# Performance work log

Hardware: AMD Instinct MI355X
Metric: run time of the kernel (lower is better)

Reference implementation:

```python
import jax, jax.numpy as jnp
import numpy as np

HEAD_DIM = 64
N_HEADS = 16
D_MODEL = 2048
SEQ = 2048
BATCH = 1
LAYER_IDX = 12
LN_EPS = 1e-5


def setup_inputs() -> dict:
    key = jax.random.key(0)
    ks = jax.random.split(key, 8)
    s = 0.02
    return {
        "x": jax.random.normal(ks[0], (BATCH, SEQ, D_MODEL), dtype=jnp.float32),
        "W_qkv": jax.random.normal(ks[1], (3 * N_HEADS * 2 * HEAD_DIM, D_MODEL), dtype=jnp.float32) * s,
        "W_o": jax.random.normal(ks[2], (D_MODEL, D_MODEL), dtype=jnp.float32) * s,
        "lambda_q1": jax.random.normal(ks[3], (2 * HEAD_DIM,), dtype=jnp.float32) * 0.1,
        "lambda_k1": jax.random.normal(ks[4], (2 * HEAD_DIM,), dtype=jnp.float32) * 0.1,
        "lambda_q2": jax.random.normal(ks[5], (2 * HEAD_DIM,), dtype=jnp.float32) * 0.1,
        "lambda_k2": jax.random.normal(ks[6], (2 * HEAD_DIM,), dtype=jnp.float32) * 0.1,
        "gn_gamma": jnp.ones((N_HEADS, 2 * HEAD_DIM), dtype=jnp.float32),
        "gn_beta": jnp.zeros((N_HEADS, 2 * HEAD_DIM), dtype=jnp.float32),
    }


def _causal_sdpa(q, k, v, scale):
    # q,k: [B,H,S,d], v: [B,H,S,2d]
    S = q.shape[2]
    scores = jnp.einsum("bhqd,bhkd->bhqk", q, k) * scale
    causal = jnp.tril(jnp.ones((S, S), dtype=bool))
    scores = jnp.where(causal[None, None], scores, jnp.float32(-1e30))
    attn = jax.nn.softmax(scores, axis=-1)
    return jnp.einsum("bhqk,bhkd->bhqd", attn, v)


def reference(x, W_qkv, W_o, lambda_q1, lambda_k1, lambda_q2, lambda_k2, gn_gamma, gn_beta):
    B, S, D = x.shape
    lambda_init = 0.8 - 0.6 * jnp.exp(jnp.float32(-0.3 * LAYER_IDX))
    scale = HEAD_DIM ** -0.5

    qkv = x @ W_qkv.T  # [B,S,6*H*d]
    qkv = qkv.reshape(B, S, 3, N_HEADS, 2 * HEAD_DIM)
    q = jnp.transpose(qkv[:, :, 0], (0, 2, 1, 3))  # [B,H,S,2d]
    k = jnp.transpose(qkv[:, :, 1], (0, 2, 1, 3))
    v = jnp.transpose(qkv[:, :, 2], (0, 2, 1, 3))
    q1, q2 = q[..., :HEAD_DIM], q[..., HEAD_DIM:]
    k1, k2 = k[..., :HEAD_DIM], k[..., HEAD_DIM:]

    lam = jnp.exp(lambda_q1 * lambda_k1) - jnp.exp(lambda_q2 * lambda_k2) + lambda_init  # [2d]

    A1 = _causal_sdpa(q1, k1, v, scale)
    A2 = _causal_sdpa(q2, k2, v, scale)
    out = A1 - lam * A2  # broadcast over value channel [B,H,S,2d]

    # per-head LayerNorm over last dim
    mu = jnp.mean(out, axis=-1, keepdims=True)
    var = jnp.mean((out - mu) ** 2, axis=-1, keepdims=True)
    out = (out - mu) * jax.lax.rsqrt(var + LN_EPS)
    out = out * gn_gamma[None, :, None, :] + gn_beta[None, :, None, :]

    out = out * (1.0 - lambda_init)
    out = jnp.transpose(out, (0, 2, 1, 3)).reshape(B, S, D)
    return out @ W_o.T
```

## Files before the change

kernel.cpp:

```cpp
#include <hip/hip_runtime.h>

typedef short short8 __attribute__((ext_vector_type(8)));
typedef float f32x4 __attribute__((ext_vector_type(4)));
typedef unsigned short u16;
typedef u16 u16x8 __attribute__((ext_vector_type(8)));
typedef u16 u16x4 __attribute__((ext_vector_type(4)));

__device__ static inline u16 f2bf(float f) {
    union { float f; unsigned u; } v; v.f = f;
    unsigned r = v.u + 0x7fffu + ((v.u >> 16) & 1u);
    return (u16)(r >> 16);
}

__global__ __launch_bounds__(256) void cast_kernel(const float* __restrict__ in,
                                                   u16* __restrict__ out, int n) {
    int i = (blockIdx.x * 256 + threadIdx.x) * 4;
    if (i + 3 < n) {
        f32x4 v = *(const f32x4*)&in[i];
        u16x4 o;
        o[0] = f2bf(v[0]); o[1] = f2bf(v[1]); o[2] = f2bf(v[2]); o[3] = f2bf(v[3]);
        *(u16x4*)&out[i] = o;
    }
}

template <int BM, int BN, int MODE, int MINW>
__global__ __launch_bounds__(256, MINW) void gemm_bt(const u16* __restrict__ A,
                                                     const u16* __restrict__ B,
                                                     int M, int N, int K,
                                                     float* __restrict__ C,
                                                     u16* __restrict__ Qo,
                                                     u16* __restrict__ Ko,
                                                     u16* __restrict__ Vo) {
    constexpr int APT = BM * 4 / 256;
    constexpr int BPT = BN * 4 / 256;
    constexpr int MT = BM / 32, NT = BN / 32;
    __shared__ u16 As[BM * 32];
    __shared__ u16 Bs[BN * 32];
    const int tid  = threadIdx.x;
    const int lane = tid & 63, wave = tid >> 6;
    const int quad = lane >> 4, l15 = lane & 15;
    const int wm = wave >> 1, wn = wave & 1;
    const int m0 = blockIdx.y * BM;
    const int n0 = blockIdx.x * BN;

    f32x4 acc[MT][NT] = {};

    const u16* aga[APT];
    const u16* bga[BPT];
#pragma unroll
    for (int i = 0; i < APT; i++) {
        int s = tid + i * 256, r = s >> 2;
        int kg = (s & 3) ^ ((r >> 1) & 3);
        aga[i] = &A[(size_t)(m0 + r) * K + kg * 8];
    }
#pragma unroll
    for (int i = 0; i < BPT; i++) {
        int s = tid + i * 256, r = s >> 2;
        int kg = (s & 3) ^ ((r >> 1) & 3);
        bga[i] = &B[(size_t)(n0 + r) * K + kg * 8];
    }

    u16x8 ast[APT], bst[BPT];
#pragma unroll
    for (int i = 0; i < APT; i++) ast[i] = *(const u16x8*)aga[i];
#pragma unroll
    for (int i = 0; i < BPT; i++) bst[i] = *(const u16x8*)bga[i];

    for (int k0 = 0; k0 < K; k0 += 32) {
        if (k0) __syncthreads();
#pragma unroll
        for (int i = 0; i < APT; i++) *(u16x8*)&As[(tid + i * 256) * 8] = ast[i];
#pragma unroll
        for (int i = 0; i < BPT; i++) *(u16x8*)&Bs[(tid + i * 256) * 8] = bst[i];
        __syncthreads();
        if (k0 + 32 < K) {
#pragma unroll
            for (int i = 0; i < APT; i++) ast[i] = *(const u16x8*)(aga[i] + k0 + 32);
#pragma unroll
            for (int i = 0; i < BPT; i++) bst[i] = *(const u16x8*)(bga[i] + k0 + 32);
        }

        short8 af[MT], bf[NT];
#pragma unroll
        for (int mt = 0; mt < MT; mt++) {
            int row = wm * (BM / 2) + mt * 16 + l15;
            int slot = row * 4 + (quad ^ ((row >> 1) & 3));
            af[mt] = *(const short8*)&As[slot * 8];
        }
#pragma unroll
        for (int nt = 0; nt < NT; nt++) {
            int row = wn * (BN / 2) + nt * 16 + l15;
            int slot = row * 4 + (quad ^ ((row >> 1) & 3));
            bf[nt] = *(const short8*)&Bs[slot * 8];
        }
#pragma unroll
        for (int mt = 0; mt < MT; mt++)
#pragma unroll
            for (int nt = 0; nt < NT; nt++)
                acc[mt][nt] = __builtin_amdgcn_mfma_f32_16x16x32_bf16(af[mt], bf[nt], acc[mt][nt], 0, 0, 0);
    }

    if (MODE == 0) {
#pragma unroll
        for (int mt = 0; mt < MT; mt++)
#pragma unroll
            for (int nt = 0; nt < NT; nt++)
#pragma unroll
                for (int r = 0; r < 4; r++) {
                    int row = m0 + wm * (BM / 2) + mt * 16 + quad * 4 + r;
                    int col = n0 + wn * (BN / 2) + nt * 16 + l15;
                    C[(size_t)row * N + col] = acc[mt][nt][r];
                }
    } else {
        const int comp = n0 >> 11, h = (n0 >> 7) & 15;
        u16* dst = (comp == 0) ? Qo : ((comp == 1) ? Ko : Vo);
        const float sc = (comp == 0) ? 0.18033688f : 1.0f;
#pragma unroll
        for (int mt = 0; mt < MT; mt++)
#pragma unroll
            for (int nt = 0; nt < NT; nt++)
#pragma unroll
                for (int r = 0; r < 4; r++) {
                    int row = m0 + wm * (BM / 2) + mt * 16 + quad * 4 + r;
                    int d = wn * (BN / 2) + nt * 16 + l15;
                    dst[((h * 2048) + row) * 128 + d] = f2bf(acc[mt][nt][r] * sc);
                }
    }
}

__global__ __launch_bounds__(256) void transpose_v(const u16* __restrict__ vb,
                                                   u16* __restrict__ vT) {
    __shared__ u16 T[64 * 136];
    const int s0 = blockIdx.x * 64, h = blockIdx.y;
    const int tid = threadIdx.x;
#pragma unroll
    for (int i = 0; i < 4; i++) {
        int c = tid + i * 256;
        int s = c >> 4, dch = c & 15;
        *(u16x8*)&T[s * 136 + dch * 8] =
            *(const u16x8*)&vb[((h * 2048) + s0 + s) * 128 + dch * 8];
    }
    __syncthreads();
#pragma unroll
    for (int i = 0; i < 4; i++) {
        int c = tid + i * 256;
        int d = c >> 3, sch = c & 7;
        u16x8 o;
#pragma unroll
        for (int j = 0; j < 8; j++) o[j] = T[(sch * 8 + j) * 136 + d];
        *(u16x8*)&vT[((h * 128) + d) * 2048 + s0 + sch * 8] = o;
    }
}

__global__ __launch_bounds__(256, 2) void attn_kernel(const u16* __restrict__ qb,
                                                      const u16* __restrict__ kb,
                                                      const u16* __restrict__ vT,
                                                      float* __restrict__ ob) {
    const int bid = blockIdx.x;
    const int h = bid & 15;
    const int comp = (bid >> 4) & 1;
    const int j = bid >> 5;
    const int J = (j < 8) ? (2 * j + 1) : (30 - 2 * j);
    const int nkt = 2 * J + 2;
    const int q0 = J * 128;
    const int tid = threadIdx.x, lane = tid & 63, wave = tid >> 6;
    const int quad = lane >> 4, l15 = lane & 15;

    __shared__ u16 Ks[64 * 64];
    __shared__ u16 VsT[128 * 64];

    const u16* kb_h = &kb[(size_t)h * 2048 * 128 + comp * 64];
    const u16* vT_h = &vT[(size_t)h * 128 * 2048];

    const int c1 = tid, c2 = tid + 256;
    const int k1key = c1 >> 3, k1dc = ((c1 & 7) ^ k1key) & 7;
    const int k2key = c2 >> 3, k2dc = ((c2 & 7) ^ k2key) & 7;
    const u16* kaddr1 = &kb_h[k1key * 128 + k1dc * 8];
    const u16* kaddr2 = &kb_h[k2key * 128 + k2dc * 8];
    const u16* vaddr[4];
#pragma unroll
    for (int i = 0; i < 4; i++) {
        int c = tid + i * 256;
        int dim = c >> 3, kc = ((c & 7) ^ dim) & 7;
        vaddr[i] = &vT_h[dim * 2048 + kc * 8];
    }

    short8 aq[2][2];
#pragma unroll
    for (int qs = 0; qs < 2; qs++)
#pragma unroll
        for (int ks = 0; ks < 2; ks++) {
            int qrow = q0 + wave * 32 + qs * 16 + l15;
            aq[qs][ks] = *(const short8*)
                &qb[((h * 2048) + qrow) * 128 + comp * 64 + ks * 32 + quad * 8];
        }

    float l_acc[2] = {0.f, 0.f};
    f32x4 acc[8][2] = {};

    u16x8 kst0, kst1, vst[4];
    kst0 = *(const u16x8*)(kaddr1);
    kst1 = *(const u16x8*)(kaddr2);
#pragma unroll
    for (int i = 0; i < 4; i++) vst[i] = *(const u16x8*)(vaddr[i]);

    for (int kt = 0; kt < nkt; kt++) {
        *(u16x8*)&Ks[c1 * 8] = kst0;
        *(u16x8*)&Ks[c2 * 8] = kst1;
#pragma unroll
        for (int i = 0; i < 4; i++) *(u16x8*)&VsT[(tid + i * 256) * 8] = vst[i];
        __syncthreads();

        if (kt + 1 < nkt) {
            const int nkt1 = kt + 1;
            kst0 = *(const u16x8*)(kaddr1 + nkt1 * 8192);
            kst1 = *(const u16x8*)(kaddr2 + nkt1 * 8192);
#pragma unroll
            for (int i = 0; i < 4; i++) vst[i] = *(const u16x8*)(vaddr[i] + nkt1 * 64);
        }

        short8 b8[2][4];
#pragma unroll
        for (int qs = 0; qs < 2; qs++) {
#pragma unroll
            for (int kn = 0; kn < 4; kn++) {
                f32x4 st = {};
#pragma unroll
                for (int ks = 0; ks < 2; ks++) {
                    int key = kn * 16 + l15;
                    int dc = ks * 4 + quad;
                    short8 kf = *(const short8*)&Ks[(key * 8 + ((dc ^ key) & 7)) * 8];
                    st = __builtin_amdgcn_mfma_f32_16x16x32_bf16(kf, aq[qs][ks], st, 0, 0, 0);
                }
                if (kt >= nkt - 2) {
                    int q = q0 + wave * 32 + qs * 16 + l15;
#pragma unroll
                    for (int r = 0; r < 4; r++) {
                        int key = kt * 64 + kn * 16 + quad * 4 + r;
                        if (key > q) st[r] = -1e30f;
                    }
                }
                float p0 = exp2f(st[0]), p1 = exp2f(st[1]);
                float p2 = exp2f(st[2]), p3 = exp2f(st[3]);
                l_acc[qs] += (p0 + p1) + (p2 + p3);
                b8[qs][kn] = short8{(short)f2bf(p0), (short)f2bf(p1),
                                    (short)f2bf(p2), (short)f2bf(p3), 0, 0, 0, 0};
            }
        }

#pragma unroll
        for (int nt = 0; nt < 8; nt++) {
            int dim = nt * 16 + l15;
#pragma unroll
            for (int kn = 0; kn < 4; kn++) {
                int g = kn * 2 + (quad >> 1);
                int sc = (g ^ dim) & 7;
                u16x4 a4 = *(const u16x4*)&VsT[dim * 64 + sc * 8 + (quad & 1) * 4];
                short8 a8 = short8{(short)a4[0], (short)a4[1], (short)a4[2], (short)a4[3],
                                   0, 0, 0, 0};
                acc[nt][0] = __builtin_amdgcn_mfma_f32_16x16x32_bf16(a8, b8[0][kn], acc[nt][0], 0, 0, 0);
                acc[nt][1] = __builtin_amdgcn_mfma_f32_16x16x32_bf16(a8, b8[1][kn], acc[nt][1], 0, 0, 0);
            }
        }
        __syncthreads();
    }

#pragma unroll
    for (int qs = 0; qs < 2; qs++) {
        l_acc[qs] += __shfl_xor(l_acc[qs], 16);
        l_acc[qs] += __shfl_xor(l_acc[qs], 32);
    }
    float rl[2] = {1.f / l_acc[0], 1.f / l_acc[1]};

#pragma unroll
    for (int qs = 0; qs < 2; qs++) {
        int s = q0 + wave * 32 + qs * 16 + l15;
        float* orow = &ob[((size_t)(comp * 16 + h) * 2048 + s) * 128 + quad * 4];
#pragma unroll
        for (int nt = 0; nt < 8; nt++) {
            f32x4 v;
#pragma unroll
            for (int r = 0; r < 4; r++) v[r] = acc[nt][qs][r] * rl[qs];
            *(f32x4*)&orow[nt * 16] = v;
        }
    }
}

__global__ __launch_bounds__(256) void combine_kernel(const float* __restrict__ ob,
                                                      const float* __restrict__ lq1,
                                                      const float* __restrict__ lk1,
                                                      const float* __restrict__ lq2,
                                                      const float* __restrict__ lk2,
                                                      const float* __restrict__ gamma,
                                                      const float* __restrict__ beta,
                                                      u16* __restrict__ attn) {
    const int tid = threadIdx.x, wave = tid >> 6, lane = tid & 63;
    const int row = blockIdx.x * 4 + wave;
    const int s = row >> 4, h = row & 15;
    const float lambda_init = 0.8f - 0.6f * __expf(-3.6f);
    const int d0 = lane * 2;
    float vals[2];
#pragma unroll
    for (int j = 0; j < 2; j++) {
        int d = d0 + j;
        float a1 = ob[((h)*2048 + s) * 128 + d];
        float a2 = ob[((16 + h) * 2048 + s) * 128 + d];
        float lam = __expf(lq1[d] * lk1[d]) - __expf(lq2[d] * lk2[d]) + lambda_init;
        vals[j] = a1 - lam * a2;
    }
    float sum = vals[0] + vals[1];
    float sq = vals[0] * vals[0] + vals[1] * vals[1];
#pragma unroll
    for (int off = 1; off < 64; off <<= 1) {
        sum += __shfl_xor(sum, off);
        sq += __shfl_xor(sq, off);
    }
    float mu = sum * (1.f / 128.f);
    float var = sq * (1.f / 128.f) - mu * mu;
    float rinv = rsqrtf(var + 1e-5f);
    float osc = 1.f - lambda_init;
#pragma unroll
    for (int j = 0; j < 2; j++) {
        int d = d0 + j;
        float g = gamma[h * 128 + d], b = beta[h * 128 + d];
        float v = ((vals[j] - mu) * rinv * g + b) * osc;
        attn[s * 2048 + h * 128 + d] = f2bf(v);
    }
}

extern "C" void kernel_launch(void* const* d_in, const int* in_sizes, int n_in,
                              void* d_out, int out_size, void* d_ws, size_t ws_size,
                              hipStream_t stream) {
    (void)in_sizes; (void)n_in; (void)out_size; (void)ws_size;
    const float* x    = (const float*)d_in[0];
    const float* Wqkv = (const float*)d_in[1];
    const float* Wo   = (const float*)d_in[2];
    const float* lq1  = (const float*)d_in[3];
    const float* lk1  = (const float*)d_in[4];
    const float* lq2  = (const float*)d_in[5];
    const float* lk2  = (const float*)d_in[6];
    const float* gam  = (const float*)d_in[7];
    const float* bet  = (const float*)d_in[8];
    float* out = (float*)d_out;

    char* ws = (char*)d_ws;
    u16*   xb    = (u16*)(ws);
    u16*   wqkvb = (u16*)(ws + (size_t)(8 << 20));
    float* ob    = (float*)(ws + (size_t)(8 << 20));
    u16*   wob   = (u16*)(ws + (size_t)(40 << 20));
    u16*   qb    = (u16*)(ws + (size_t)(48 << 20));
    u16*   kb    = (u16*)(ws + (size_t)(56 << 20));
    u16*   vb    = (u16*)(ws + (size_t)(64 << 20));
    u16*   vT    = (u16*)(ws + (size_t)(72 << 20));
    u16*   attn  = (u16*)(ws);

    cast_kernel<<<(2048 * 2048) / 1024, 256, 0, stream>>>(x, xb, 2048 * 2048);
    cast_kernel<<<(6144 * 2048) / 1024, 256, 0, stream>>>(Wqkv, wqkvb, 6144 * 2048);
    cast_kernel<<<(2048 * 2048) / 1024, 256, 0, stream>>>(Wo, wob, 2048 * 2048);
    gemm_bt<128, 128, 1, 3><<<dim3(48, 16), 256, 0, stream>>>(
        xb, wqkvb, 2048, 6144, 2048, nullptr, qb, kb, vb);
    transpose_v<<<dim3(32, 16), 256, 0, stream>>>(vb, vT);
    attn_kernel<<<512, 256, 0, stream>>>(qb, kb, vT, ob);
    combine_kernel<<<8192, 256, 0, stream>>>(ob, lq1, lk1, lq2, lk2, gam, bet, attn);
    gemm_bt<128, 64, 0, 2><<<dim3(32, 16), 256, 0, stream>>>(
        attn, wob, 2048, 2048, 2048, out, nullptr, nullptr, nullptr);
}
```

Baseline: 295.5 us.

## Pack two key blocks per PV MFMA to halve zero-padded matrix ops

The PV product previously issued MFMA 16x16x32 with half the K operand zero-padded. Now two 16-key score blocks are packed into one full 32-wide operand, which halves the PV MFMA count. Probabilities are converted with the packed hardware bf16 instruction, K fragments are hoisted with precomputed LDS offsets, and the PV phase runs at raised wave priority. The value fragment gather must match the new key ordering, and the precomputed offsets add register pressure.

```diff
diff --git a/kernel.cpp b/kernel.cpp
--- a/kernel.cpp
+++ b/kernel.cpp
@@ -10,6 +10,12 @@
     union { float f; unsigned u; } v; v.f = f;
     unsigned r = v.u + 0x7fffu + ((v.u >> 16) & 1u);
     return (u16)(r >> 16);
+}
+
+__device__ static inline unsigned cvt_pk_bf16(float a, float b) {
+    unsigned r;
+    asm("v_cvt_pk_bf16_f32 %0, %1, %2" : "=v"(r) : "v"(a), "v"(b));
+    return r;
 }
 
 __global__ __launch_bounds__(256) void cast_kernel(const float* __restrict__ in,
@@ -165,9 +171,12 @@
     const int q0 = J * 128;
     const int tid = threadIdx.x, lane = tid & 63, wave = tid >> 6;
     const int quad = lane >> 4, l15 = lane & 15;
+    const int qh = quad >> 1, ql = quad & 1;
 
     __shared__ u16 Ks[64 * 64];
     __shared__ u16 VsT[128 * 64];
+    const char* KsB = (const char*)Ks;
+    const char* VsB = (const char*)VsT;
 
     const u16* kb_h = &kb[(size_t)h * 2048 * 128 + comp * 64];
     const u16* vT_h = &vT[(size_t)h * 128 * 2048];
@@ -185,6 +194,17 @@
         vaddr[i] = &vT_h[dim * 2048 + kc * 8];
     }
 
+    const int koff0 = l15 * 128 + ((quad ^ l15) & 7) * 16;
+    const int koff1 = l15 * 128 + (((quad + 4) ^ l15) & 7) * 16;
+    int vb[8][2];
+#pragma unroll
+    for (int nt = 0; nt < 8; nt++) {
+        int dim = nt * 16 + l15;
+        int base = dim * 128 + ((qh ^ dim) & 7) * 16 + ql * 8;
+        vb[nt][0] = base;
+        vb[nt][1] = base ^ 64;
+    }
+
     short8 aq[2][2];
 #pragma unroll
     for (int qs = 0; qs < 2; qs++)
@@ -199,10 +219,15 @@
     f32x4 acc[8][2] = {};
 
     u16x8 kst0, kst1, vst[4];
-    kst0 = *(const u16x8*)(kaddr1);
-    kst1 = *(const u16x8*)(kaddr2);
-#pragma unroll
-    for (int i = 0; i < 4; i++) vst[i] = *(const u16x8*)(vaddr[i]);
+    kst0 = *(const u16x8*)kaddr1;
+    kst1 = *(const u16x8*)kaddr2;
+#pragma unroll
+    for (int i = 0; i < 4; i++) vst[i] = *(const u16x8*)vaddr[i];
+    const u16* kp1 = kaddr1 + 8192;
+    const u16* kp2 = kaddr2 + 8192;
+    const u16* vp[4];
+#pragma unroll
+    for (int i = 0; i < 4; i++) vp[i] = vaddr[i] + 64;
 
     for (int kt = 0; kt < nkt; kt++) {
         *(u16x8*)&Ks[c1 * 8] = kst0;
@@ -212,56 +237,64 @@
         __syncthreads();
 
         if (kt + 1 < nkt) {
-            const int nkt1 = kt + 1;
-            kst0 = *(const u16x8*)(kaddr1 + nkt1 * 8192);
-            kst1 = *(const u16x8*)(kaddr2 + nkt1 * 8192);
-#pragma unroll
-            for (int i = 0; i < 4; i++) vst[i] = *(const u16x8*)(vaddr[i] + nkt1 * 64);
-        }
-
-        short8 b8[2][4];
+            kst0 = *(const u16x8*)kp1; kp1 += 8192;
+            kst1 = *(const u16x8*)kp2; kp2 += 8192;
+#pragma unroll
+            for (int i = 0; i < 4; i++) { vst[i] = *(const u16x8*)vp[i]; vp[i] += 64; }
+        }
+
+        short8 kf[4][2];
+#pragma unroll
+        for (int kn = 0; kn < 4; kn++) {
+            kf[kn][0] = *(const short8*)(KsB + (koff0 + kn * 2048));
+            kf[kn][1] = *(const short8*)(KsB + (koff1 + kn * 2048));
+        }
+
+        short8 b8[2][2];
 #pragma unroll
         for (int qs = 0; qs < 2; qs++) {
 #pragma unroll
-            for (int kn = 0; kn < 4; kn++) {
-                f32x4 st = {};
-#pragma unroll
-                for (int ks = 0; ks < 2; ks++) {
-                    int key = kn * 16 + l15;
-                    int dc = ks * 4 + quad;
-                    short8 kf = *(const short8*)&Ks[(key * 8 + ((dc ^ key) & 7)) * 8];
-                    st = __builtin_amdgcn_mfma_f32_16x16x32_bf16(kf, aq[qs][ks], st, 0, 0, 0);
-                }
+            for (int kn2 = 0; kn2 < 2; kn2++) {
+                f32x4 sa = {}, sb = {};
+                sa = __builtin_amdgcn_mfma_f32_16x16x32_bf16(kf[2 * kn2][0], aq[qs][0], sa, 0, 0, 0);
+                sa = __builtin_amdgcn_mfma_f32_16x16x32_bf16(kf[2 * kn2][1], aq[qs][1], sa, 0, 0, 0);
+                sb = __builtin_amdgcn_mfma_f32_16x16x32_bf16(kf[2 * kn2 + 1][0], aq[qs][0], sb, 0, 0, 0);
+                sb = __builtin_amdgcn_mfma_f32_16x16x32_bf16(kf[2 * kn2 + 1][1], aq[qs][1], sb, 0, 0, 0);
                 if (kt >= nkt - 2) {
                     int q = q0 + wave * 32 + qs * 16 + l15;
+                    int kb0 = kt * 64 + kn2 * 32 + quad * 4;
 #pragma unroll
                     for (int r = 0; r < 4; r++) {
-                        int key = kt * 64 + kn * 16 + quad * 4 + r;
-                        if (key > q) st[r] = -1e30f;
+                        if (kb0 + r > q) sa[r] = -1e30f;
+                        if (kb0 + 16 + r > q) sb[r] = -1e30f;
                     }
                 }
-                float p0 = exp2f(st[0]), p1 = exp2f(st[1]);
-                float p2 = exp2f(st[2]), p3 = exp2f(st[3]);
-                l_acc[qs] += (p0 + p1) + (p2 + p3);
-                b8[qs][kn] = short8{(short)f2bf(p0), (short)f2bf(p1),
-                                    (short)f2bf(p2), (short)f2bf(p3), 0, 0, 0, 0};
+                float p0 = exp2f(sa[0]), p1 = exp2f(sa[1]), p2 = exp2f(sa[2]), p3 = exp2f(sa[3]);
+                float p4 = exp2f(sb[0]), p5 = exp2f(sb[1]), p6 = exp2f(sb[2]), p7 = exp2f(sb[3]);
+                l_acc[qs] += ((p0 + p1) + (p2 + p3)) + ((p4 + p5) + (p6 + p7));
+                union { unsigned w[4]; short8 s; } pw;
+                pw.w[0] = cvt_pk_bf16(p0, p1);
+                pw.w[1] = cvt_pk_bf16(p2, p3);
+                pw.w[2] = cvt_pk_bf16(p4, p5);
+                pw.w[3] = cvt_pk_bf16(p6, p7);
+                b8[qs][kn2] = pw.s;
             }
         }
 
+        __builtin_amdgcn_s_setprio(1);
 #pragma unroll
         for (int nt = 0; nt < 8; nt++) {
-            int dim = nt * 16 + l15;
-#pragma unroll
-            for (int kn = 0; kn < 4; kn++) {
-                int g = kn * 2 + (quad >> 1);
-                int sc = (g ^ dim) & 7;
-                u16x4 a4 = *(const u16x4*)&VsT[dim * 64 + sc * 8 + (quad & 1) * 4];
-                short8 a8 = short8{(short)a4[0], (short)a4[1], (short)a4[2], (short)a4[3],
-                                   0, 0, 0, 0};
-                acc[nt][0] = __builtin_amdgcn_mfma_f32_16x16x32_bf16(a8, b8[0][kn], acc[nt][0], 0, 0, 0);
-                acc[nt][1] = __builtin_amdgcn_mfma_f32_16x16x32_bf16(a8, b8[1][kn], acc[nt][1], 0, 0, 0);
+#pragma unroll
+            for (int kn2 = 0; kn2 < 2; kn2++) {
+                union { u16x4 h4[2]; short8 s; } av;
+                int o0 = vb[nt][kn2];
+                av.h4[0] = *(const u16x4*)(VsB + o0);
+                av.h4[1] = *(const u16x4*)(VsB + (o0 ^ 32));
+                acc[nt][0] = __builtin_amdgcn_mfma_f32_16x16x32_bf16(av.s, b8[0][kn2], acc[nt][0], 0, 0, 0);
+                acc[nt][1] = __builtin_amdgcn_mfma_f32_16x16x32_bf16(av.s, b8[1][kn2], acc[nt][1], 0, 0, 0);
             }
         }
+        __builtin_amdgcn_s_setprio(0);
         __syncthreads();
     }
 
```

Result: faster. 286.7 us (-3.0%).
